# Performance work log

Hardware: AMD Instinct MI355X
Metric: run time of the kernel (lower is better)

Reference implementation:

```python
import jax, jax.numpy as jnp
import numpy as np

B, S, IN, OUT, R, E = 8, 2048, 4096, 4096, 16, 64
ALPHA = 1.0


def setup_inputs() -> dict:
    ks = jax.random.split(jax.random.key(0), 7)
    return {
        "x": jax.random.normal(ks[0], (B, S, IN), jnp.float32),
        "query_signal": jax.random.normal(ks[1], (B, IN), jnp.float32),
        "A_pool": jax.random.normal(ks[2], (E, R, IN), jnp.float32),
        # original inits B pool to zeros; use small random values for a non-degenerate baseline
        "B_pool": jax.random.normal(ks[3], (E, OUT, R), jnp.float32) * 0.02,
        "W_rA": jax.random.normal(ks[4], (E, IN), jnp.float32) * 0.02,
        "b_rA": jnp.zeros((E,), jnp.float32),
        "W_rB": jax.random.normal(ks[5], (E, IN), jnp.float32) * 0.02,
        "b_rB": jnp.zeros((E,), jnp.float32),
        "cfs_W": jax.random.normal(ks[6], (R, IN, E), jnp.float32),
    }


def reference(x, query_signal, A_pool, B_pool, W_rA, b_rA, W_rB, b_rB, cfs_W):
    ranks = jnp.arange(R)  # rank slot k pairs with the k-th top-k expert index
    # IFS router A -> top-r expert indices per sample
    g_A_scores = query_signal @ W_rA.T + b_rA            # (B, E)
    _, idx_A = jax.lax.top_k(g_A_scores, R)              # (B, R)
    # gather: k-th selected expert contributes its k-th rank row
    lora_A = A_pool[idx_A, ranks[None, :], :]            # (B, R, IN)
    # router B scores: IFS linear + CFS content score (detached lora_A)
    g_B_scores = (query_signal @ W_rB.T + b_rB
                  + jnp.einsum('bri,rie->be', jax.lax.stop_gradient(lora_A), cfs_W))  # (B, E)
    _, idx_B = jax.lax.top_k(g_B_scores, R)              # (B, R)
    lora_B = jnp.transpose(B_pool, (0, 2, 1))[idx_B, ranks[None, :], :]  # (B, R, OUT)
    # two batched low-rank matmuls
    after_A = jnp.einsum('bsi,bri->bsr', x, lora_A)      # (B, S, R)
    lora_delta = jnp.einsum('bsr,bro->bso', after_A, lora_B)  # (B, S, OUT)
    return lora_delta * ALPHA
```

## Files before the change

kernel.cpp:

```cpp
#include <hip/hip_runtime.h>

#define B_ 8
#define S_ 2048
#define IN_ 4096
#define OUT_ 4096
#define R_ 16
#define E_ 64

typedef float v4f __attribute__((ext_vector_type(4)));

__device__ __forceinline__ float4 ntload4(const float* p) {
  v4f t = __builtin_nontemporal_load((const v4f*)p);
  float4 r; r.x = t.x; r.y = t.y; r.z = t.z; r.w = t.w; return r;
}
__device__ __forceinline__ void ntstore4(float* p, float4 v) {
  v4f t; t.x = v.x; t.y = v.y; t.z = v.z; t.w = v.w;
  __builtin_nontemporal_store(t, (v4f*)p);
}

__device__ __forceinline__ float dot4(float4 a, float4 b) {
  return a.x*b.x + a.y*b.y + a.z*b.z + a.w*b.w;
}

__device__ __forceinline__ void topk16(float v, int* __restrict__ dst) {
  const int lane = threadIdx.x & 63;
  for (int r = 0; r < R_; ++r) {
    float mv = v; int mi = lane;
    #pragma unroll
    for (int off = 1; off < 64; off <<= 1) {
      float v2 = __shfl_xor(mv, off, 64);
      int   i2 = __shfl_xor(mi, off, 64);
      if (v2 > mv || (v2 == mv && i2 < mi)) { mv = v2; mi = i2; }
    }
    if (lane == 0) dst[r] = mi;
    if (lane == mi) v = -__builtin_inff();
  }
}

__global__ __launch_bounds__(256) void k_scores(
    const float* __restrict__ q, const float* __restrict__ W_rA,
    const float* __restrict__ W_rB, float* __restrict__ sApart,
    float* __restrict__ gApart)
{
  const int bx = blockIdx.x;
  const int b = bx >> 5, eg = (bx >> 2) & 7, ic = bx & 3;
  __shared__ float qs[1024];
  const int tid = threadIdx.x;
  {
    const float4* q4 = (const float4*)(q + (size_t)b * IN_ + ic * 1024);
    ((float4*)qs)[tid] = q4[tid];
  }
  __syncthreads();
  const int wave = tid >> 6, lane = tid & 63;
  const float4* qs4 = (const float4*)qs;
  #pragma unroll
  for (int k = 0; k < 2; ++k) {
    const int e = eg * 8 + wave * 2 + k;
    const float4* wa = (const float4*)(W_rA + (size_t)e * IN_ + ic * 1024);
    const float4* wb = (const float4*)(W_rB + (size_t)e * IN_ + ic * 1024);
    float pa = 0.f, pb = 0.f;
    #pragma unroll
    for (int i = 0; i < 4; ++i) {
      float4 qv = qs4[lane + i * 64];
      pa += dot4(qv, wa[lane + i * 64]);
      pb += dot4(qv, wb[lane + i * 64]);
    }
    #pragma unroll
    for (int off = 1; off < 64; off <<= 1) {
      pa += __shfl_xor(pa, off, 64);
      pb += __shfl_xor(pb, off, 64);
    }
    if (lane == 0) {
      sApart[(ic * B_ + b) * E_ + e] = pa;
      gApart[(ic * B_ + b) * E_ + e] = pb;
    }
  }
}

__global__ __launch_bounds__(64) void k_topk_a(
    const float* __restrict__ sApart, const float* __restrict__ gApart,
    const float* __restrict__ b_rA, const float* __restrict__ b_rB,
    float* __restrict__ gB0, int* __restrict__ idxA)
{
  const int b = blockIdx.x;
  const int e = threadIdx.x & 63;
  float sA = b_rA[e], g = b_rB[e];
  #pragma unroll
  for (int ic = 0; ic < 4; ++ic) {
    sA += sApart[(ic * B_ + b) * E_ + e];
    g  += gApart[(ic * B_ + b) * E_ + e];
  }
  gB0[b * E_ + e] = g;
  topk16(sA, idxA + b * R_);
}

__global__ __launch_bounds__(256) void k_fused_ac(
    const float* __restrict__ x, const float* __restrict__ A_pool,
    const int* __restrict__ idxA, const float* __restrict__ cfs,
    float* __restrict__ gBpart, float* __restrict__ partial)
{
  __shared__ union {
    struct { float4 As[R_][128]; float aa[64][R_]; } a;
    struct { float as[B_][512]; float red[4][B_][E_]; } c;
  } sm;
  const int tid = threadIdx.x;

  if (blockIdx.x < 128) {
    const int blk = blockIdx.x;
    const int r = blk >> 3, ic = blk & 7;
    {
      const int b = tid >> 5, t = tid & 31;
      const int e = idxA[b * R_ + r];
      const float4* src = (const float4*)(A_pool + ((size_t)e * R_ + r) * IN_ + ic * 512);
      float4* dst = (float4*)sm.c.as[b];
      for (int j = t; j < 128; j += 32) dst[j] = src[j];
    }
    __syncthreads();
    const int e = tid & 63, part = tid >> 6;
    float acc[B_];
    #pragma unroll
    for (int b = 0; b < B_; ++b) acc[b] = 0.f;
    const float* cbase = cfs + ((size_t)r * IN_ + ic * 512) * E_ + e;
    for (int i = part * 128; i < part * 128 + 128; ++i) {
      float c = __builtin_nontemporal_load(cbase + (size_t)i * E_);
      #pragma unroll
      for (int b = 0; b < B_; ++b) acc[b] += sm.c.as[b][i] * c;
    }
    #pragma unroll
    for (int b = 0; b < B_; ++b) sm.c.red[part][b][e] = acc[b];
    __syncthreads();
    if (tid < 64) {
      #pragma unroll
      for (int b = 0; b < B_; ++b)
        gBpart[((size_t)blk * B_ + b) * E_ + tid] =
            sm.c.red[0][b][tid] + sm.c.red[1][b][tid] +
            sm.c.red[2][b][tid] + sm.c.red[3][b][tid];
    }
    return;
  }

  const int bx = blockIdx.x - 128;
  const int rt = bx & 31, b = (bx >> 5) & 7, ks = bx >> 8;
  const int row0 = rt * 64;
  {
    const int sr = tid >> 4, st = tid & 15;
    const float4* src =
        (const float4*)(A_pool + ((size_t)idxA[b * R_ + sr] * R_ + sr) * IN_ + ks * 512);
    #pragma unroll
    for (int j = st; j < 128; j += 16) sm.a.As[sr][j] = src[j];
  }
  const int rg = tid >> 4, p = tid & 15;
  const float* xbase = x + ((size_t)b * S_ + row0 + rg * 4) * IN_ + ks * 512;
  float acc[4][R_];
  #pragma unroll
  for (int m = 0; m < 4; ++m)
    #pragma unroll
    for (int r = 0; r < R_; ++r) acc[m][r] = 0.f;
  __syncthreads();

  #pragma unroll 2
  for (int step = 0; step < 8; ++step) {
    const int i4 = step * 16 + p;
    float4 xv[4];
    #pragma unroll
    for (int m = 0; m < 4; ++m)
      xv[m] = ntload4(xbase + (size_t)m * IN_ + i4 * 4);
    #pragma unroll
    for (int r = 0; r < R_; ++r) {
      float4 a = sm.a.As[r][i4];
      #pragma unroll
      for (int m = 0; m < 4; ++m) acc[m][r] += dot4(xv[m], a);
    }
  }
  #pragma unroll
  for (int m = 0; m < 4; ++m)
    #pragma unroll
    for (int r = 0; r < R_; ++r) {
      float v = acc[m][r];
      v += __shfl_xor(v, 1, 64);
      v += __shfl_xor(v, 2, 64);
      v += __shfl_xor(v, 4, 64);
      v += __shfl_xor(v, 8, 64);
      acc[m][r] = v;
    }
  if (p == 0) {
    #pragma unroll
    for (int m = 0; m < 4; ++m) {
      float4* d4 = (float4*)sm.a.aa[rg * 4 + m];
      d4[0] = make_float4(acc[m][0],  acc[m][1],  acc[m][2],  acc[m][3]);
      d4[1] = make_float4(acc[m][4],  acc[m][5],  acc[m][6],  acc[m][7]);
      d4[2] = make_float4(acc[m][8],  acc[m][9],  acc[m][10], acc[m][11]);
      d4[3] = make_float4(acc[m][12], acc[m][13], acc[m][14], acc[m][15]);
    }
  }
  __syncthreads();
  float4 w = ((const float4*)sm.a.aa)[tid];
  ntstore4(partial + (((size_t)(b * 32 + rt) * 8 + ks) << 10) + tid * 4, w);
}

__global__ __launch_bounds__(256) void k_topkb_pack(
    const float* __restrict__ gB0, const float* __restrict__ gBpart,
    const float* __restrict__ B_pool, float* __restrict__ loraBp)
{
  const int b = blockIdx.x >> 4, r = blockIdx.x & 15;
  __shared__ float red[4][E_];
  __shared__ int idxB_s[R_];
  const int tid = threadIdx.x;
  const int wave = tid >> 6, lane = tid & 63;
  float p = 0.f;
  for (int blk = wave * 32; blk < wave * 32 + 32; ++blk)
    p += gBpart[((size_t)blk * B_ + b) * E_ + lane];
  red[wave][lane] = p;
  __syncthreads();
  if (wave == 0) {
    float v = gB0[b * E_ + lane] + red[0][lane] + red[1][lane] + red[2][lane] + red[3][lane];
    topk16(v, idxB_s);
  }
  __syncthreads();
  const int e = idxB_s[r];
  const float* src = B_pool + (size_t)e * OUT_ * R_ + r;
  float* dst = loraBp + (size_t)(b * R_ + r) * OUT_;
  #pragma unroll
  for (int i = 0; i < 16; ++i) {
    const int o = i * 256 + tid;
    dst[o] = src[(size_t)o * R_];
  }
}

__global__ __launch_bounds__(256) void k_out(
    const float* __restrict__ partial, const float* __restrict__ loraBp,
    float* __restrict__ out)
{
  const int bx = blockIdx.x;
  const int oc = bx & 3, st = (bx >> 2) & 63, b = bx >> 8;
  __shared__ float aa[32][R_];
  const int tid = threadIdx.x;
  if (tid < 128) {
    const float* base = partial + (((size_t)(b * 32 + (st >> 1)) * 8) << 10)
                        + (st & 1) * 512 + tid * 4;
    float4 s = ntload4(base);
    #pragma unroll
    for (int k = 1; k < 8; ++k) {
      float4 t = ntload4(base + k * 1024);
      s.x += t.x; s.y += t.y; s.z += t.z; s.w += t.w;
    }
    ((float4*)aa)[tid] = s;
  }
  float4 Bf[R_];
  #pragma unroll
  for (int r = 0; r < R_; ++r)
    Bf[r] = *(const float4*)(loraBp + (size_t)(b * R_ + r) * OUT_ + oc * 1024 + tid * 4);
  __syncthreads();
  const int row0 = st * 32;
  float* obase = out + ((size_t)b * S_ + row0) * OUT_ + oc * 1024 + tid * 4;
  #pragma unroll 2
  for (int s = 0; s < 32; ++s) {
    const float4* av = (const float4*)aa[s];
    float4 a0 = av[0], a1 = av[1], a2 = av[2], a3 = av[3];
    float4 o = make_float4(0.f, 0.f, 0.f, 0.f);
    o.x += a0.x*Bf[0].x;  o.y += a0.x*Bf[0].y;  o.z += a0.x*Bf[0].z;  o.w += a0.x*Bf[0].w;
    o.x += a0.y*Bf[1].x;  o.y += a0.y*Bf[1].y;  o.z += a0.y*Bf[1].z;  o.w += a0.y*Bf[1].w;
    o.x += a0.z*Bf[2].x;  o.y += a0.z*Bf[2].y;  o.z += a0.z*Bf[2].z;  o.w += a0.z*Bf[2].w;
    o.x += a0.w*Bf[3].x;  o.y += a0.w*Bf[3].y;  o.z += a0.w*Bf[3].z;  o.w += a0.w*Bf[3].w;
    o.x += a1.x*Bf[4].x;  o.y += a1.x*Bf[4].y;  o.z += a1.x*Bf[4].z;  o.w += a1.x*Bf[4].w;
    o.x += a1.y*Bf[5].x;  o.y += a1.y*Bf[5].y;  o.z += a1.y*Bf[5].z;  o.w += a1.y*Bf[5].w;
    o.x += a1.z*Bf[6].x;  o.y += a1.z*Bf[6].y;  o.z += a1.z*Bf[6].z;  o.w += a1.z*Bf[6].w;
    o.x += a1.w*Bf[7].x;  o.y += a1.w*Bf[7].y;  o.z += a1.w*Bf[7].z;  o.w += a1.w*Bf[7].w;
    o.x += a2.x*Bf[8].x;  o.y += a2.x*Bf[8].y;  o.z += a2.x*Bf[8].z;  o.w += a2.x*Bf[8].w;
    o.x += a2.y*Bf[9].x;  o.y += a2.y*Bf[9].y;  o.z += a2.y*Bf[9].z;  o.w += a2.y*Bf[9].w;
    o.x += a2.z*Bf[10].x; o.y += a2.z*Bf[10].y; o.z += a2.z*Bf[10].z; o.w += a2.z*Bf[10].w;
    o.x += a2.w*Bf[11].x; o.y += a2.w*Bf[11].y; o.z += a2.w*Bf[11].z; o.w += a2.w*Bf[11].w;
    o.x += a3.x*Bf[12].x; o.y += a3.x*Bf[12].y; o.z += a3.x*Bf[12].z; o.w += a3.x*Bf[12].w;
    o.x += a3.y*Bf[13].x; o.y += a3.y*Bf[13].y; o.z += a3.y*Bf[13].z; o.w += a3.y*Bf[13].w;
    o.x += a3.z*Bf[14].x; o.y += a3.z*Bf[14].y; o.z += a3.z*Bf[14].z; o.w += a3.z*Bf[14].w;
    o.x += a3.w*Bf[15].x; o.y += a3.w*Bf[15].y; o.z += a3.w*Bf[15].z; o.w += a3.w*Bf[15].w;
    ntstore4(obase + (size_t)s * OUT_, o);
  }
}

extern "C" void kernel_launch(void* const* d_in, const int* in_sizes, int n_in,
                              void* d_out, int out_size, void* d_ws, size_t ws_size,
                              hipStream_t stream) {
  const float* x      = (const float*)d_in[0];
  const float* qsig   = (const float*)d_in[1];
  const float* A_pool = (const float*)d_in[2];
  const float* B_pool = (const float*)d_in[3];
  const float* W_rA   = (const float*)d_in[4];
  const float* b_rA   = (const float*)d_in[5];
  const float* W_rB   = (const float*)d_in[6];
  const float* b_rB   = (const float*)d_in[7];
  const float* cfs_W  = (const float*)d_in[8];
  float* out = (float*)d_out;

  char* w = (char*)d_ws;
  int*   idxA    = (int*)(w);
  float* sApart  = (float*)(w + 1024);
  float* gApart  = (float*)(w + 9216);
  float* gB0     = (float*)(w + 17408);
  float* gBpart  = (float*)(w + 19456);
  float* loraBp  = (float*)(w + 281600);
  float* partial = (float*)(w + 2378752);

  k_scores<<<256, 256, 0, stream>>>(qsig, W_rA, W_rB, sApart, gApart);
  k_topk_a<<<8, 64, 0, stream>>>(sApart, gApart, b_rA, b_rB, gB0, idxA);
  k_fused_ac<<<2176, 256, 0, stream>>>(x, A_pool, idxA, cfs_W, gBpart, partial);
  k_topkb_pack<<<128, 256, 0, stream>>>(gB0, gBpart, B_pool, loraBp);
  k_out<<<2048, 256, 0, stream>>>(partial, loraBp, out);
}
```

Baseline: 175.1 us.

## Fuse x·A projection with output expansion and split CFS scoring into own kernel

Each block now computes the rank-16 projection for 32 rows across the full input dimension and then writes the output tile directly. This removes the partial-sum buffer and the separate output kernel. The CFS router scoring moves to a standalone kernel that runs before the top-k pack, so it no longer overlaps with the x streaming. The grid shrinks to 512 blocks, which reduces parallelism and latency hiding for the bandwidth-bound x reads.

```diff
diff --git a/kernel.cpp b/kernel.cpp
--- a/kernel.cpp
+++ b/kernel.cpp
@@ -94,86 +94,121 @@
   topk16(sA, idxA + b * R_);
 }
 
-__global__ __launch_bounds__(256) void k_fused_ac(
+__global__ __launch_bounds__(256) void k_cfs(
+    const float* __restrict__ A_pool, const float* __restrict__ cfs,
+    const int* __restrict__ idxA, float* __restrict__ gBpart)
+{
+  const int blk = blockIdx.x;
+  const int r = blk >> 4, ic = blk & 15;
+  __shared__ float as[B_][256];
+  __shared__ float red[4][B_][E_];
+  const int tid = threadIdx.x;
+  {
+    const int b = tid >> 5, t = tid & 31;
+    const int e = idxA[b * R_ + r];
+    const float4* src = (const float4*)(A_pool + ((size_t)e * R_ + r) * IN_ + ic * 256);
+    float4* dst = (float4*)as[b];
+    for (int j = t; j < 64; j += 32) dst[j] = src[j];
+  }
+  __syncthreads();
+  const int e = tid & 63, part = tid >> 6;
+  float acc[B_];
+  #pragma unroll
+  for (int b = 0; b < B_; ++b) acc[b] = 0.f;
+  const float* cbase = cfs + ((size_t)r * IN_ + ic * 256) * E_ + e;
+  for (int i = part * 64; i < part * 64 + 64; ++i) {
+    float c = __builtin_nontemporal_load(cbase + (size_t)i * E_);
+    #pragma unroll
+    for (int b = 0; b < B_; ++b) acc[b] += as[b][i] * c;
+  }
+  #pragma unroll
+  for (int b = 0; b < B_; ++b) red[part][b][e] = acc[b];
+  __syncthreads();
+  if (tid < 64) {
+    #pragma unroll
+    for (int b = 0; b < B_; ++b)
+      gBpart[((size_t)blk * B_ + b) * E_ + tid] =
+          red[0][b][tid] + red[1][b][tid] + red[2][b][tid] + red[3][b][tid];
+  }
+}
+
+__global__ __launch_bounds__(256) void k_topkb_pack(
+    const float* __restrict__ gB0, const float* __restrict__ gBpart,
+    const float* __restrict__ B_pool, float* __restrict__ loraBp)
+{
+  const int b = blockIdx.x >> 4, r = blockIdx.x & 15;
+  __shared__ float red[4][E_];
+  __shared__ int idxB_s[R_];
+  const int tid = threadIdx.x;
+  const int wave = tid >> 6, lane = tid & 63;
+  float p = 0.f;
+  for (int blk = wave * 64; blk < wave * 64 + 64; ++blk)
+    p += gBpart[((size_t)blk * B_ + b) * E_ + lane];
+  red[wave][lane] = p;
+  __syncthreads();
+  if (wave == 0) {
+    float v = gB0[b * E_ + lane] + red[0][lane] + red[1][lane] + red[2][lane] + red[3][lane];
+    topk16(v, idxB_s);
+  }
+  __syncthreads();
+  const int e = idxB_s[r];
+  const float* src = B_pool + (size_t)e * OUT_ * R_ + r;
+  float* dst = loraBp + (size_t)(b * R_ + r) * OUT_;
+  #pragma unroll
+  for (int i = 0; i < 16; ++i) {
+    const int o = i * 256 + tid;
+    dst[o] = src[(size_t)o * R_];
+  }
+}
+
+__global__ __launch_bounds__(256) void k_fused_ao(
     const float* __restrict__ x, const float* __restrict__ A_pool,
-    const int* __restrict__ idxA, const float* __restrict__ cfs,
-    float* __restrict__ gBpart, float* __restrict__ partial)
-{
-  __shared__ union {
-    struct { float4 As[R_][128]; float aa[64][R_]; } a;
-    struct { float as[B_][512]; float red[4][B_][E_]; } c;
-  } sm;
-  const int tid = threadIdx.x;
-
-  if (blockIdx.x < 128) {
-    const int blk = blockIdx.x;
-    const int r = blk >> 3, ic = blk & 7;
+    const int* __restrict__ idxA, const float* __restrict__ loraBp,
+    float* __restrict__ out)
+{
+  const int bx = blockIdx.x;
+  const int b = bx >> 6, rt = bx & 63;
+  const int row0 = rt * 32;
+  __shared__ float4 As[R_][128];
+  __shared__ float aa[32][R_];
+  const int tid = threadIdx.x;
+  const int sr = tid >> 4, stt = tid & 15;
+  const size_t arow = ((size_t)idxA[b * R_ + sr] * R_ + sr) * IN_;
+  const int rg = tid >> 4, p = tid & 15;
+  const float* xrow = x + ((size_t)b * S_ + row0 + rg * 2) * IN_;
+
+  float acc[2][R_];
+  #pragma unroll
+  for (int m = 0; m < 2; ++m)
+    #pragma unroll
+    for (int r = 0; r < R_; ++r) acc[m][r] = 0.f;
+
+  for (int ks = 0; ks < 8; ++ks) {
+    if (ks) __syncthreads();
     {
-      const int b = tid >> 5, t = tid & 31;
-      const int e = idxA[b * R_ + r];
-      const float4* src = (const float4*)(A_pool + ((size_t)e * R_ + r) * IN_ + ic * 512);
-      float4* dst = (float4*)sm.c.as[b];
-      for (int j = t; j < 128; j += 32) dst[j] = src[j];
+      const float4* src = (const float4*)(A_pool + arow + ks * 512);
+      #pragma unroll
+      for (int j = stt; j < 128; j += 16) As[sr][j] = src[j];
     }
     __syncthreads();
-    const int e = tid & 63, part = tid >> 6;
-    float acc[B_];
-    #pragma unroll
-    for (int b = 0; b < B_; ++b) acc[b] = 0.f;
-    const float* cbase = cfs + ((size_t)r * IN_ + ic * 512) * E_ + e;
-    for (int i = part * 128; i < part * 128 + 128; ++i) {
-      float c = __builtin_nontemporal_load(cbase + (size_t)i * E_);
+    const float* xbase = xrow + ks * 512;
+    #pragma unroll 2
+    for (int step = 0; step < 8; ++step) {
+      const int i4 = step * 16 + p;
+      float4 xv[2];
       #pragma unroll
-      for (int b = 0; b < B_; ++b) acc[b] += sm.c.as[b][i] * c;
-    }
-    #pragma unroll
-    for (int b = 0; b < B_; ++b) sm.c.red[part][b][e] = acc[b];
-    __syncthreads();
-    if (tid < 64) {
+      for (int m = 0; m < 2; ++m)
+        xv[m] = ntload4(xbase + (size_t)m * IN_ + (size_t)i4 * 4);
       #pragma unroll
-      for (int b = 0; b < B_; ++b)
-        gBpart[((size_t)blk * B_ + b) * E_ + tid] =
-            sm.c.red[0][b][tid] + sm.c.red[1][b][tid] +
-            sm.c.red[2][b][tid] + sm.c.red[3][b][tid];
-    }
-    return;
-  }
-
-  const int bx = blockIdx.x - 128;
-  const int rt = bx & 31, b = (bx >> 5) & 7, ks = bx >> 8;
-  const int row0 = rt * 64;
-  {
-    const int sr = tid >> 4, st = tid & 15;
-    const float4* src =
-        (const float4*)(A_pool + ((size_t)idxA[b * R_ + sr] * R_ + sr) * IN_ + ks * 512);
-    #pragma unroll
-    for (int j = st; j < 128; j += 16) sm.a.As[sr][j] = src[j];
-  }
-  const int rg = tid >> 4, p = tid & 15;
-  const float* xbase = x + ((size_t)b * S_ + row0 + rg * 4) * IN_ + ks * 512;
-  float acc[4][R_];
-  #pragma unroll
-  for (int m = 0; m < 4; ++m)
-    #pragma unroll
-    for (int r = 0; r < R_; ++r) acc[m][r] = 0.f;
-  __syncthreads();
-
-  #pragma unroll 2
-  for (int step = 0; step < 8; ++step) {
-    const int i4 = step * 16 + p;
-    float4 xv[4];
-    #pragma unroll
-    for (int m = 0; m < 4; ++m)
-      xv[m] = ntload4(xbase + (size_t)m * IN_ + i4 * 4);
-    #pragma unroll
-    for (int r = 0; r < R_; ++r) {
-      float4 a = sm.a.As[r][i4];
-      #pragma unroll
-      for (int m = 0; m < 4; ++m) acc[m][r] += dot4(xv[m], a);
-    }
-  }
-  #pragma unroll
-  for (int m = 0; m < 4; ++m)
+      for (int r = 0; r < R_; ++r) {
+        float4 a = As[r][i4];
+        #pragma unroll
+        for (int m = 0; m < 2; ++m) acc[m][r] += dot4(xv[m], a);
+      }
+    }
+  }
+  #pragma unroll
+  for (int m = 0; m < 2; ++m)
     #pragma unroll
     for (int r = 0; r < R_; ++r) {
       float v = acc[m][r];
@@ -185,8 +220,8 @@
     }
   if (p == 0) {
     #pragma unroll
-    for (int m = 0; m < 4; ++m) {
-      float4* d4 = (float4*)sm.a.aa[rg * 4 + m];
+    for (int m = 0; m < 2; ++m) {
+      float4* d4 = (float4*)aa[rg * 2 + m];
       d4[0] = make_float4(acc[m][0],  acc[m][1],  acc[m][2],  acc[m][3]);
       d4[1] = make_float4(acc[m][4],  acc[m][5],  acc[m][6],  acc[m][7]);
       d4[2] = make_float4(acc[m][8],  acc[m][9],  acc[m][10], acc[m][11]);
@@ -194,87 +229,37 @@
     }
   }
   __syncthreads();
-  float4 w = ((const float4*)sm.a.aa)[tid];
-  ntstore4(partial + (((size_t)(b * 32 + rt) * 8 + ks) << 10) + tid * 4, w);
-}
-
-__global__ __launch_bounds__(256) void k_topkb_pack(
-    const float* __restrict__ gB0, const float* __restrict__ gBpart,
-    const float* __restrict__ B_pool, float* __restrict__ loraBp)
-{
-  const int b = blockIdx.x >> 4, r = blockIdx.x & 15;
-  __shared__ float red[4][E_];
-  __shared__ int idxB_s[R_];
-  const int tid = threadIdx.x;
-  const int wave = tid >> 6, lane = tid & 63;
-  float p = 0.f;
-  for (int blk = wave * 32; blk < wave * 32 + 32; ++blk)
-    p += gBpart[((size_t)blk * B_ + b) * E_ + lane];
-  red[wave][lane] = p;
-  __syncthreads();
-  if (wave == 0) {
-    float v = gB0[b * E_ + lane] + red[0][lane] + red[1][lane] + red[2][lane] + red[3][lane];
-    topk16(v, idxB_s);
-  }
-  __syncthreads();
-  const int e = idxB_s[r];
-  const float* src = B_pool + (size_t)e * OUT_ * R_ + r;
-  float* dst = loraBp + (size_t)(b * R_ + r) * OUT_;
-  #pragma unroll
-  for (int i = 0; i < 16; ++i) {
-    const int o = i * 256 + tid;
-    dst[o] = src[(size_t)o * R_];
-  }
-}
-
-__global__ __launch_bounds__(256) void k_out(
-    const float* __restrict__ partial, const float* __restrict__ loraBp,
-    float* __restrict__ out)
-{
-  const int bx = blockIdx.x;
-  const int oc = bx & 3, st = (bx >> 2) & 63, b = bx >> 8;
-  __shared__ float aa[32][R_];
-  const int tid = threadIdx.x;
-  if (tid < 128) {
-    const float* base = partial + (((size_t)(b * 32 + (st >> 1)) * 8) << 10)
-                        + (st & 1) * 512 + tid * 4;
-    float4 s = ntload4(base);
-    #pragma unroll
-    for (int k = 1; k < 8; ++k) {
-      float4 t = ntload4(base + k * 1024);
-      s.x += t.x; s.y += t.y; s.z += t.z; s.w += t.w;
-    }
-    ((float4*)aa)[tid] = s;
-  }
-  float4 Bf[R_];
-  #pragma unroll
-  for (int r = 0; r < R_; ++r)
-    Bf[r] = *(const float4*)(loraBp + (size_t)(b * R_ + r) * OUT_ + oc * 1024 + tid * 4);
-  __syncthreads();
-  const int row0 = st * 32;
-  float* obase = out + ((size_t)b * S_ + row0) * OUT_ + oc * 1024 + tid * 4;
-  #pragma unroll 2
-  for (int s = 0; s < 32; ++s) {
-    const float4* av = (const float4*)aa[s];
-    float4 a0 = av[0], a1 = av[1], a2 = av[2], a3 = av[3];
-    float4 o = make_float4(0.f, 0.f, 0.f, 0.f);
-    o.x += a0.x*Bf[0].x;  o.y += a0.x*Bf[0].y;  o.z += a0.x*Bf[0].z;  o.w += a0.x*Bf[0].w;
-    o.x += a0.y*Bf[1].x;  o.y += a0.y*Bf[1].y;  o.z += a0.y*Bf[1].z;  o.w += a0.y*Bf[1].w;
-    o.x += a0.z*Bf[2].x;  o.y += a0.z*Bf[2].y;  o.z += a0.z*Bf[2].z;  o.w += a0.z*Bf[2].w;
-    o.x += a0.w*Bf[3].x;  o.y += a0.w*Bf[3].y;  o.z += a0.w*Bf[3].z;  o.w += a0.w*Bf[3].w;
-    o.x += a1.x*Bf[4].x;  o.y += a1.x*Bf[4].y;  o.z += a1.x*Bf[4].z;  o.w += a1.x*Bf[4].w;
-    o.x += a1.y*Bf[5].x;  o.y += a1.y*Bf[5].y;  o.z += a1.y*Bf[5].z;  o.w += a1.y*Bf[5].w;
-    o.x += a1.z*Bf[6].x;  o.y += a1.z*Bf[6].y;  o.z += a1.z*Bf[6].z;  o.w += a1.z*Bf[6].w;
-    o.x += a1.w*Bf[7].x;  o.y += a1.w*Bf[7].y;  o.z += a1.w*Bf[7].z;  o.w += a1.w*Bf[7].w;
-    o.x += a2.x*Bf[8].x;  o.y += a2.x*Bf[8].y;  o.z += a2.x*Bf[8].z;  o.w += a2.x*Bf[8].w;
-    o.x += a2.y*Bf[9].x;  o.y += a2.y*Bf[9].y;  o.z += a2.y*Bf[9].z;  o.w += a2.y*Bf[9].w;
-    o.x += a2.z*Bf[10].x; o.y += a2.z*Bf[10].y; o.z += a2.z*Bf[10].z; o.w += a2.z*Bf[10].w;
-    o.x += a2.w*Bf[11].x; o.y += a2.w*Bf[11].y; o.z += a2.w*Bf[11].z; o.w += a2.w*Bf[11].w;
-    o.x += a3.x*Bf[12].x; o.y += a3.x*Bf[12].y; o.z += a3.x*Bf[12].z; o.w += a3.x*Bf[12].w;
-    o.x += a3.y*Bf[13].x; o.y += a3.y*Bf[13].y; o.z += a3.y*Bf[13].z; o.w += a3.y*Bf[13].w;
-    o.x += a3.z*Bf[14].x; o.y += a3.z*Bf[14].y; o.z += a3.z*Bf[14].z; o.w += a3.z*Bf[14].w;
-    o.x += a3.w*Bf[15].x; o.y += a3.w*Bf[15].y; o.z += a3.w*Bf[15].z; o.w += a3.w*Bf[15].w;
-    ntstore4(obase + (size_t)s * OUT_, o);
+
+  #pragma unroll
+  for (int oc = 0; oc < 4; ++oc) {
+    float4 Bf[R_];
+    #pragma unroll
+    for (int r = 0; r < R_; ++r)
+      Bf[r] = *(const float4*)(loraBp + (size_t)(b * R_ + r) * OUT_ + oc * 1024 + tid * 4);
+    float* obase = out + ((size_t)b * S_ + row0) * OUT_ + oc * 1024 + tid * 4;
+    #pragma unroll 2
+    for (int s = 0; s < 32; ++s) {
+      const float4* av = (const float4*)aa[s];
+      float4 a0 = av[0], a1 = av[1], a2 = av[2], a3 = av[3];
+      float4 o = make_float4(0.f, 0.f, 0.f, 0.f);
+      o.x += a0.x*Bf[0].x;  o.y += a0.x*Bf[0].y;  o.z += a0.x*Bf[0].z;  o.w += a0.x*Bf[0].w;
+      o.x += a0.y*Bf[1].x;  o.y += a0.y*Bf[1].y;  o.z += a0.y*Bf[1].z;  o.w += a0.y*Bf[1].w;
+      o.x += a0.z*Bf[2].x;  o.y += a0.z*Bf[2].y;  o.z += a0.z*Bf[2].z;  o.w += a0.z*Bf[2].w;
+      o.x += a0.w*Bf[3].x;  o.y += a0.w*Bf[3].y;  o.z += a0.w*Bf[3].z;  o.w += a0.w*Bf[3].w;
+      o.x += a1.x*Bf[4].x;  o.y += a1.x*Bf[4].y;  o.z += a1.x*Bf[4].z;  o.w += a1.x*Bf[4].w;
+      o.x += a1.y*Bf[5].x;  o.y += a1.y*Bf[5].y;  o.z += a1.y*Bf[5].z;  o.w += a1.y*Bf[5].w;
+      o.x += a1.z*Bf[6].x;  o.y += a1.z*Bf[6].y;  o.z += a1.z*Bf[6].z;  o.w += a1.z*Bf[6].w;
+      o.x += a1.w*Bf[7].x;  o.y += a1.w*Bf[7].y;  o.z += a1.w*Bf[7].z;  o.w += a1.w*Bf[7].w;
+      o.x += a2.x*Bf[8].x;  o.y += a2.x*Bf[8].y;  o.z += a2.x*Bf[8].z;  o.w += a2.x*Bf[8].w;
+      o.x += a2.y*Bf[9].x;  o.y += a2.y*Bf[9].y;  o.z += a2.y*Bf[9].z;  o.w += a2.y*Bf[9].w;
+      o.x += a2.z*Bf[10].x; o.y += a2.z*Bf[10].y; o.z += a2.z*Bf[10].z; o.w += a2.z*Bf[10].w;
+      o.x += a2.w*Bf[11].x; o.y += a2.w*Bf[11].y; o.z += a2.w*Bf[11].z; o.w += a2.w*Bf[11].w;
+      o.x += a3.x*Bf[12].x; o.y += a3.x*Bf[12].y; o.z += a3.x*Bf[12].z; o.w += a3.x*Bf[12].w;
+      o.x += a3.y*Bf[13].x; o.y += a3.y*Bf[13].y; o.z += a3.y*Bf[13].z; o.w += a3.y*Bf[13].w;
+      o.x += a3.z*Bf[14].x; o.y += a3.z*Bf[14].y; o.z += a3.z*Bf[14].z; o.w += a3.z*Bf[14].w;
+      o.x += a3.w*Bf[15].x; o.y += a3.w*Bf[15].y; o.z += a3.w*Bf[15].z; o.w += a3.w*Bf[15].w;
+      ntstore4(obase + (size_t)s * OUT_, o);
+    }
   }
 }
 
@@ -298,12 +283,11 @@
   float* gApart  = (float*)(w + 9216);
   float* gB0     = (float*)(w + 17408);
   float* gBpart  = (float*)(w + 19456);
-  float* loraBp  = (float*)(w + 281600);
-  float* partial = (float*)(w + 2378752);
+  float* loraBp  = (float*)(w + 543744);
 
   k_scores<<<256, 256, 0, stream>>>(qsig, W_rA, W_rB, sApart, gApart);
   k_topk_a<<<8, 64, 0, stream>>>(sApart, gApart, b_rA, b_rB, gB0, idxA);
-  k_fused_ac<<<2176, 256, 0, stream>>>(x, A_pool, idxA, cfs_W, gBpart, partial);
+  k_cfs<<<256, 256, 0, stream>>>(A_pool, cfs_W, idxA, gBpart);
   k_topkb_pack<<<128, 256, 0, stream>>>(gB0, gBpart, B_pool, loraBp);
-  k_out<<<2048, 256, 0, stream>>>(partial, loraBp, out);
-}
+  k_fused_ao<<<512, 256, 0, stream>>>(x, A_pool, idxA, loraBp, out);
+}
```

Measured after the change: 213.6 us. +22.0%, slower.

## Restructure x·A tile so each thread owns one row, half the K slice

Applied to the files above, without the earlier changes.

The x·lora_A stage now gives each thread one sequence row and half of a 512-wide K slice, and each block covers 128 rows instead of 64. This removes the 16-lane shuffle reduction and the shared-memory staging of results, leaving a single pairwise shuffle. Partial sums are written in a new (ks, b, s, r) layout that the output kernel reads with a matching stride. In exchange, x loads become per-thread strided rows that are no longer coalesced across the wavefront, and they drop the nontemporal hint, which may hurt memory efficiency on the dominant 1 GB stream of x.

```diff
diff --git a/kernel.cpp b/kernel.cpp
--- a/kernel.cpp
+++ b/kernel.cpp
@@ -100,7 +100,7 @@
     float* __restrict__ gBpart, float* __restrict__ partial)
 {
   __shared__ union {
-    struct { float4 As[R_][128]; float aa[64][R_]; } a;
+    struct { float4 As[R_][128]; } a;
     struct { float as[B_][512]; float red[4][B_][E_]; } c;
   } sm;
   const int tid = threadIdx.x;
@@ -140,62 +140,40 @@
   }
 
   const int bx = blockIdx.x - 128;
-  const int rt = bx & 31, b = (bx >> 5) & 7, ks = bx >> 8;
-  const int row0 = rt * 64;
+  const int rt = bx & 15, b = (bx >> 4) & 7, ks = bx >> 7;
   {
-    const int sr = tid >> 4, st = tid & 15;
+    const int sr = tid >> 4, stt = tid & 15;
     const float4* src =
         (const float4*)(A_pool + ((size_t)idxA[b * R_ + sr] * R_ + sr) * IN_ + ks * 512);
     #pragma unroll
-    for (int j = st; j < 128; j += 16) sm.a.As[sr][j] = src[j];
-  }
-  const int rg = tid >> 4, p = tid & 15;
-  const float* xbase = x + ((size_t)b * S_ + row0 + rg * 4) * IN_ + ks * 512;
-  float acc[4][R_];
-  #pragma unroll
-  for (int m = 0; m < 4; ++m)
-    #pragma unroll
-    for (int r = 0; r < R_; ++r) acc[m][r] = 0.f;
-  __syncthreads();
-
-  #pragma unroll 2
-  for (int step = 0; step < 8; ++step) {
-    const int i4 = step * 16 + p;
-    float4 xv[4];
-    #pragma unroll
-    for (int m = 0; m < 4; ++m)
-      xv[m] = ntload4(xbase + (size_t)m * IN_ + i4 * 4);
-    #pragma unroll
-    for (int r = 0; r < R_; ++r) {
-      float4 a = sm.a.As[r][i4];
-      #pragma unroll
-      for (int m = 0; m < 4; ++m) acc[m][r] += dot4(xv[m], a);
-    }
-  }
-  #pragma unroll
-  for (int m = 0; m < 4; ++m)
-    #pragma unroll
-    for (int r = 0; r < R_; ++r) {
-      float v = acc[m][r];
-      v += __shfl_xor(v, 1, 64);
-      v += __shfl_xor(v, 2, 64);
-      v += __shfl_xor(v, 4, 64);
-      v += __shfl_xor(v, 8, 64);
-      acc[m][r] = v;
-    }
-  if (p == 0) {
-    #pragma unroll
-    for (int m = 0; m < 4; ++m) {
-      float4* d4 = (float4*)sm.a.aa[rg * 4 + m];
-      d4[0] = make_float4(acc[m][0],  acc[m][1],  acc[m][2],  acc[m][3]);
-      d4[1] = make_float4(acc[m][4],  acc[m][5],  acc[m][6],  acc[m][7]);
-      d4[2] = make_float4(acc[m][8],  acc[m][9],  acc[m][10], acc[m][11]);
-      d4[3] = make_float4(acc[m][12], acc[m][13], acc[m][14], acc[m][15]);
-    }
-  }
-  __syncthreads();
-  float4 w = ((const float4*)sm.a.aa)[tid];
-  ntstore4(partial + (((size_t)(b * 32 + rt) * 8 + ks) << 10) + tid * 4, w);
+    for (int j = stt; j < 128; j += 16) sm.a.As[sr][j] = src[j];
+  }
+  const int j = tid >> 1, h = tid & 1;
+  const int row = rt * 128 + j;
+  const float* xbase = x + ((size_t)b * S_ + row) * IN_ + ks * 512 + h * 256;
+  float acc[R_];
+  #pragma unroll
+  for (int r = 0; r < R_; ++r) acc[r] = 0.f;
+  __syncthreads();
+
+  const float4* As4 = &sm.a.As[0][0] + h * 64;
+  #pragma unroll 4
+  for (int i4 = 0; i4 < 64; ++i4) {
+    float4 xv = *(const float4*)(xbase + (size_t)i4 * 4);
+    #pragma unroll
+    for (int r = 0; r < R_; ++r)
+      acc[r] += dot4(xv, As4[r * 128 + i4]);
+  }
+  #pragma unroll
+  for (int r = 0; r < R_; ++r)
+    acc[r] += __shfl_xor(acc[r], 1, 64);
+  if (h == 0) {
+    float* dst = partial + (((size_t)(ks * B_ + b) * S_) + row) * R_;
+    ntstore4(dst + 0,  make_float4(acc[0],  acc[1],  acc[2],  acc[3]));
+    ntstore4(dst + 4,  make_float4(acc[4],  acc[5],  acc[6],  acc[7]));
+    ntstore4(dst + 8,  make_float4(acc[8],  acc[9],  acc[10], acc[11]));
+    ntstore4(dst + 12, make_float4(acc[12], acc[13], acc[14], acc[15]));
+  }
 }
 
 __global__ __launch_bounds__(256) void k_topkb_pack(
@@ -236,12 +214,12 @@
   __shared__ float aa[32][R_];
   const int tid = threadIdx.x;
   if (tid < 128) {
-    const float* base = partial + (((size_t)(b * 32 + (st >> 1)) * 8) << 10)
-                        + (st & 1) * 512 + tid * 4;
+    const float* base = partial + ((size_t)b * S_ + st * 32) * R_ + tid * 4;
+    const size_t kstride = (size_t)B_ * S_ * R_;
     float4 s = ntload4(base);
     #pragma unroll
     for (int k = 1; k < 8; ++k) {
-      float4 t = ntload4(base + k * 1024);
+      float4 t = ntload4(base + k * kstride);
       s.x += t.x; s.y += t.y; s.z += t.z; s.w += t.w;
     }
     ((float4*)aa)[tid] = s;
@@ -303,7 +281,7 @@
 
   k_scores<<<256, 256, 0, stream>>>(qsig, W_rA, W_rB, sApart, gApart);
   k_topk_a<<<8, 64, 0, stream>>>(sApart, gApart, b_rA, b_rB, gB0, idxA);
-  k_fused_ac<<<2176, 256, 0, stream>>>(x, A_pool, idxA, cfs_W, gBpart, partial);
+  k_fused_ac<<<1152, 256, 0, stream>>>(x, A_pool, idxA, cfs_W, gBpart, partial);
   k_topkb_pack<<<128, 256, 0, stream>>>(gB0, gBpart, B_pool, loraBp);
   k_out<<<2048, 256, 0, stream>>>(partial, loraBp, out);
 }
```

New measurement: 184.6 us. +5.4%, slower.
